# Performance work log

Measured on AMD Instinct MI355X. Metric: run time of the kernel, lower is better.

The kernel has to match this reference:

```python
import jax, jax.numpy as jnp
import numpy as np

EPS = 1e-6
H, A, V = 4, 64, 64  # heads, attn_dim, hidden_dim


def layer_norm(x, w, b):
    mu = jnp.mean(x, axis=-1, keepdims=True)
    var = jnp.var(x, axis=-1, keepdims=True)
    return (x - mu) * jax.lax.rsqrt(var + EPS) * w + b


def setup_inputs() -> dict:
    key = jax.random.key(0)
    B, N, D = 4, 2048, 512
    lengths = np.array([2048, 1536, 1024, 1792], np.int32)
    offsets = np.concatenate([[0], np.cumsum(lengths)]).astype(np.int32)
    L = int(offsets[-1])  # 6400
    uvqk_out = (2 * V + 2 * A) * H  # 1024
    out_in = 2 * V * H + D          # concat([u, x, normed_attn])
    ks = jax.random.split(key, 4)
    return {
        "x": jax.random.normal(ks[0], (L, D), jnp.float32),
        "x_lengths": jnp.asarray(lengths),
        "x_offsets": jnp.asarray(offsets),
        "max_seq_len": N,
        "num_targets": jnp.asarray([32, 16, 8, 64], jnp.int32),
        "uvqk_weight": jax.random.normal(ks[1], (D, uvqk_out), jnp.float32) / np.float32(np.sqrt(D)),
        "uvqk_bias": jnp.zeros((uvqk_out,), jnp.float32),
        "input_norm_weight": jnp.ones((D,), jnp.float32),
        "input_norm_bias": jnp.zeros((D,), jnp.float32),
        "output_norm_weight": jnp.ones((V * H,), jnp.float32),
        "output_norm_bias": jnp.zeros((V * H,), jnp.float32),
        "output_weight": jax.random.normal(ks[2], (out_in, D), jnp.float32) / np.float32(np.sqrt(out_in)),
    }


def reference(x, x_lengths, x_offsets, max_seq_len, num_targets,
              uvqk_weight, uvqk_bias, input_norm_weight, input_norm_bias,
              output_norm_weight, output_norm_bias, output_weight):
    L, D = x.shape
    B = x_lengths.shape[0]
    N = int(max_seq_len)
    alpha = A ** -0.5

    # fused input layernorm + UVQK projection + silu
    nx = layer_norm(x, input_norm_weight, input_norm_bias)
    uvqk = jax.nn.silu(nx @ uvqk_weight + uvqk_bias)              # [L, (2V+2A)*H]
    u = uvqk[:, : V * H]                                          # [L, V*H]
    v = uvqk[:, V * H: 2 * V * H].reshape(L, H, V)
    q = uvqk[:, 2 * V * H: 2 * V * H + A * H].reshape(L, H, A)
    k = uvqk[:, 2 * V * H + A * H:].reshape(L, H, A)

    # jagged -> padded [B, N, ...]
    pos = jnp.arange(N)
    gather_idx = jnp.clip(x_offsets[:-1, None] + pos[None, :], 0, L - 1)  # [B,N]
    valid = pos[None, :] < x_lengths[:, None]                              # [B,N]
    qp = q[gather_idx] * valid[..., None, None]
    kp = k[gather_idx] * valid[..., None, None]
    vp = v[gather_idx] * valid[..., None, None]

    # target-aware causal mask: clamp ids at uih boundary; eye | dist>0
    max_ids = (x_lengths - num_targets)[:, None]        # [B,1]
    ids = jnp.minimum(pos[None, :], max_ids)            # [B,N]
    dist = ids[:, :, None] - ids[:, None, :]            # [B,N,N]
    mask = (dist > 0) | jnp.eye(N, dtype=bool)[None]
    mask = mask & valid[:, :, None] & valid[:, None, :]

    scores = jnp.einsum("bnha,bmha->bhnm", qp, kp) * alpha
    attn_w = jax.nn.silu(scores) * (1.0 / N)
    attn_w = attn_w * mask[:, None].astype(attn_w.dtype)
    attn_p = jnp.einsum("bhnm,bmhv->bnhv", attn_w, vp).reshape(B, N, H * V)

    # padded -> jagged
    tok = jnp.arange(L)
    b_of = jnp.searchsorted(x_offsets, tok, side="right") - 1
    p_of = tok - x_offsets[b_of]
    attn = attn_p[b_of, p_of]                            # [L, H*V]

    # output: norm(attn), concat [u, x, y], project, residual (dropout off / eval)
    y = layer_norm(attn, output_norm_weight, output_norm_bias)
    y = jnp.concatenate([u, x, y], axis=1)
    return x + y @ output_weight
```

## Files before the change

kernel.cpp:

```cpp
#include <hip/hip_runtime.h>
#include <math.h>

#define NSEQ 2048
#define PIT 72
#define GP 40

typedef __attribute__((ext_vector_type(8))) short short8;
typedef __attribute__((ext_vector_type(4))) short short4v;
typedef __attribute__((ext_vector_type(4))) float f32x4;

__device__ __forceinline__ float silu_f(float z) {
    return z * __builtin_amdgcn_rcpf(1.f + __expf(-z));
}

__device__ __forceinline__ unsigned short f2bf(float f) {
    unsigned int u = __float_as_uint(f);
    u += 0x7fffu + ((u >> 16) & 1u);
    return (unsigned short)(u >> 16);
}

__device__ __forceinline__ unsigned short f2bf_fast(float f) {
    return (unsigned short)((__float_as_uint(f) + 0x8000u) >> 16);
}

__device__ __forceinline__ short8 scale8_pow2(short8 v, float s) {
    short8 r;
    #pragma unroll
    for (int i = 0; i < 8; i++) {
        float f = __uint_as_float(((unsigned int)(unsigned short)v[i]) << 16) * s;
        r[i] = (short)(unsigned short)(__float_as_uint(f) >> 16);
    }
    return r;
}

__global__ void __launch_bounds__(256) transpose_to_bf16(
    const float* __restrict__ W, unsigned short* __restrict__ Wt, int R, int C)
{
    __shared__ float t[32][33];
    int tid = threadIdx.x;
    int tr = tid >> 5, tc = tid & 31;
    int r0 = blockIdx.y * 32, c0 = blockIdx.x * 32;
    #pragma unroll
    for (int p = 0; p < 4; p++)
        t[tr + p * 8][tc] = W[(size_t)(r0 + tr + p * 8) * C + c0 + tc];
    __syncthreads();
    #pragma unroll
    for (int p = 0; p < 4; p++)
        Wt[(size_t)(c0 + tr + p * 8) * R + r0 + tc] = f2bf(t[tc][tr + p * 8]);
}

__global__ void __launch_bounds__(256) ln512_kernel(
    const float* __restrict__ x, const float* __restrict__ w,
    const float* __restrict__ b,
    unsigned short* __restrict__ nxb, unsigned short* __restrict__ A2)
{
    int row = blockIdx.x;
    int tid = threadIdx.x;
    const float* xr = x + (size_t)row * 512;
    float2 v = *(const float2*)(xr + tid * 2);
    float s = v.x + v.y;
    float sq = v.x * v.x + v.y * v.y;
    for (int o = 32; o > 0; o >>= 1) { s += __shfl_down(s, o); sq += __shfl_down(sq, o); }
    __shared__ float red[8];
    int wv = tid >> 6;
    if ((tid & 63) == 0) { red[wv] = s; red[4 + wv] = sq; }
    __syncthreads();
    float ts = red[0] + red[1] + red[2] + red[3];
    float tq = red[4] + red[5] + red[6] + red[7];
    float mu = ts * (1.f / 512.f);
    float var = tq * (1.f / 512.f) - mu * mu;
    float rs = rsqrtf(var + 1e-6f);
    float2 wv2 = *(const float2*)(w + tid * 2);
    float2 bv  = *(const float2*)(b + tid * 2);
    ushort2 hn, hx;
    hn.x = f2bf((v.x - mu) * rs * wv2.x + bv.x);
    hn.y = f2bf((v.y - mu) * rs * wv2.y + bv.y);
    hx.x = f2bf(v.x);
    hx.y = f2bf(v.y);
    *(ushort2*)(nxb + (size_t)row * 512 + tid * 2) = hn;
    *(ushort2*)(A2 + (size_t)row * 1024 + 256 + tid * 2) = hx;
}

__global__ void __launch_bounds__(256) ln256_kernel(
    const float* __restrict__ a, const float* __restrict__ w,
    const float* __restrict__ b, unsigned short* __restrict__ A2)
{
    int row = blockIdx.x;
    int tid = threadIdx.x;
    float v = a[(size_t)row * 256 + tid];
    float s = v, sq = v * v;
    for (int o = 32; o > 0; o >>= 1) { s += __shfl_down(s, o); sq += __shfl_down(sq, o); }
    __shared__ float red[8];
    int wv = tid >> 6;
    if ((tid & 63) == 0) { red[wv] = s; red[4 + wv] = sq; }
    __syncthreads();
    float ts = red[0] + red[1] + red[2] + red[3];
    float tq = red[4] + red[5] + red[6] + red[7];
    float mu = ts * (1.f / 256.f);
    float var = tq * (1.f / 256.f) - mu * mu;
    float rs = rsqrtf(var + 1e-6f);
    A2[(size_t)row * 1024 + 768 + tid] = f2bf((v - mu) * rs * w[tid] + b[tid]);
}

__global__ void __launch_bounds__(256) gemm1_mfma(
    const unsigned short* __restrict__ Ab, const unsigned short* __restrict__ Bt,
    const float* __restrict__ bias,
    unsigned short* __restrict__ A2, unsigned short* __restrict__ qkvb)
{
    constexpr int K = 512, KIT = K / 32;
    __shared__ unsigned short As[2][128 * GP];
    __shared__ unsigned short Bs[2][64 * GP];
    int tid = threadIdx.x, lane = tid & 63, w = tid >> 6;
    int nn = lane & 15, qd = lane >> 4;
    int bm = blockIdx.y * 128, bn = blockIdx.x * 64;
    int arow = tid >> 1, aseg = (tid & 1) * 16;
    int brow = tid >> 2, bseg = (tid & 3) * 8;
    const unsigned short* Ag = Ab + (size_t)(bm + arow) * K + aseg;
    const unsigned short* Bg = Bt + (size_t)(bn + brow) * K + bseg;

    short8 pa0 = *(const short8*)Ag;
    short8 pa1 = *(const short8*)(Ag + 8);
    short8 pb0 = *(const short8*)Bg;

    f32x4 acc[2][4];
    #pragma unroll
    for (int i = 0; i < 2; i++)
        #pragma unroll
        for (int j = 0; j < 4; j++) acc[i][j] = (f32x4){0.f, 0.f, 0.f, 0.f};

    int buf = 0;
    for (int it = 0; it < KIT; ++it) {
        *(short8*)&As[buf][arow * GP + aseg]     = pa0;
        *(short8*)&As[buf][arow * GP + aseg + 8] = pa1;
        *(short8*)&Bs[buf][brow * GP + bseg]     = pb0;
        __syncthreads();
        if (it + 1 < KIT) {
            int k0 = (it + 1) * 32;
            pa0 = *(const short8*)(Ag + k0);
            pa1 = *(const short8*)(Ag + k0 + 8);
            pb0 = *(const short8*)(Bg + k0);
        }
        short8 af[2], bf[4];
        #pragma unroll
        for (int i = 0; i < 2; i++)
            af[i] = *(const short8*)&As[buf][(w * 32 + i * 16 + nn) * GP + qd * 8];
        #pragma unroll
        for (int j = 0; j < 4; j++)
            bf[j] = *(const short8*)&Bs[buf][(j * 16 + nn) * GP + qd * 8];
        #pragma unroll
        for (int i = 0; i < 2; i++)
            #pragma unroll
            for (int j = 0; j < 4; j++)
                acc[i][j] = __builtin_amdgcn_mfma_f32_16x16x32_bf16(af[i], bf[j], acc[i][j], 0, 0, 0);
        buf ^= 1;
    }
    bool isU = (bn < 256);
    #pragma unroll
    for (int j = 0; j < 4; j++) {
        int col = bn + j * 16 + nn;
        float bb = bias[col];
        #pragma unroll
        for (int i = 0; i < 2; i++) {
            int rbase = bm + w * 32 + i * 16 + qd * 4;
            #pragma unroll
            for (int r = 0; r < 4; r++) {
                unsigned short hh = f2bf(silu_f(acc[i][j][r] + bb));
                if (isU) A2[(size_t)(rbase + r) * 1024 + col] = hh;
                else     qkvb[(size_t)(rbase + r) * 768 + col - 256] = hh;
            }
        }
    }
}

__global__ void __launch_bounds__(256) gemm2_mfma(
    const unsigned short* __restrict__ Ab, const unsigned short* __restrict__ Bt,
    const float* __restrict__ x, float* __restrict__ out)
{
    constexpr int K = 1024, KIT = K / 32;
    __shared__ unsigned short As[2][128 * GP];
    __shared__ unsigned short Bs[2][64 * GP];
    int tid = threadIdx.x, lane = tid & 63, w = tid >> 6;
    int nn = lane & 15, qd = lane >> 4;
    int bm = blockIdx.y * 128, bn = blockIdx.x * 64;
    int arow = tid >> 1, aseg = (tid & 1) * 16;
    int brow = tid >> 2, bseg = (tid & 3) * 8;
    const unsigned short* Ag = Ab + (size_t)(bm + arow) * K + aseg;
    const unsigned short* Bg = Bt + (size_t)(bn + brow) * K + bseg;

    short8 pa0 = *(const short8*)Ag;
    short8 pa1 = *(const short8*)(Ag + 8);
    short8 pb0 = *(const short8*)Bg;

    f32x4 acc[2][4];
    #pragma unroll
    for (int i = 0; i < 2; i++)
        #pragma unroll
        for (int j = 0; j < 4; j++) acc[i][j] = (f32x4){0.f, 0.f, 0.f, 0.f};

    int buf = 0;
    for (int it = 0; it < KIT; ++it) {
        *(short8*)&As[buf][arow * GP + aseg]     = pa0;
        *(short8*)&As[buf][arow * GP + aseg + 8] = pa1;
        *(short8*)&Bs[buf][brow * GP + bseg]     = pb0;
        __syncthreads();
        if (it + 1 < KIT) {
            int k0 = (it + 1) * 32;
            pa0 = *(const short8*)(Ag + k0);
            pa1 = *(const short8*)(Ag + k0 + 8);
            pb0 = *(const short8*)(Bg + k0);
        }
        short8 af[2], bf[4];
        #pragma unroll
        for (int i = 0; i < 2; i++)
            af[i] = *(const short8*)&As[buf][(w * 32 + i * 16 + nn) * GP + qd * 8];
        #pragma unroll
        for (int j = 0; j < 4; j++)
            bf[j] = *(const short8*)&Bs[buf][(j * 16 + nn) * GP + qd * 8];
        #pragma unroll
        for (int i = 0; i < 2; i++)
            #pragma unroll
            for (int j = 0; j < 4; j++)
                acc[i][j] = __builtin_amdgcn_mfma_f32_16x16x32_bf16(af[i], bf[j], acc[i][j], 0, 0, 0);
        buf ^= 1;
    }
    #pragma unroll
    for (int j = 0; j < 4; j++) {
        int col = bn + j * 16 + nn;
        #pragma unroll
        for (int i = 0; i < 2; i++) {
            int rbase = bm + w * 32 + i * 16 + qd * 4;
            #pragma unroll
            for (int r = 0; r < 4; r++) {
                size_t idx = (size_t)(rbase + r) * 512 + col;
                out[idx] = x[idx] + acc[i][j][r];
            }
        }
    }
}

__global__ void __launch_bounds__(256, 2) attn_mfma_kernel(
    const unsigned short* __restrict__ qkvb,
    const int* __restrict__ offsets,
    const int* __restrict__ lengths,
    const int* __restrict__ num_targets,
    float* __restrict__ attn)
{
    int bh = blockIdx.y;
    int b = bh >> 2, h = bh & 3;
    int len = lengths[b];
    int n0 = (31 - (int)blockIdx.x) * 64;
    if (n0 >= len) return;
    int m_hi = min(n0 + 63, len - 1);
    int off = offsets[b];
    int max_id = len - num_targets[b];
    int tid = threadIdx.x, lane = tid & 63, w = tid >> 6;
    int nn = lane & 15, qd = lane >> 4;

    __shared__ __align__(16) char smem[69632];
    unsigned short* Vt = (unsigned short*)(smem + w * 9216);
    float* Os = (float*)smem;

    short8 qf[4][2];
    #pragma unroll
    for (int g = 0; g < 4; g++) {
        int row = min(n0 + g * 16 + nn, len - 1);
        const unsigned short* base = qkvb + (size_t)(off + row) * 768 + 256 + h * 64;
        qf[g][0] = scale8_pow2(*(const short8*)(base + qd * 8), 0.125f);
        qf[g][1] = scale8_pow2(*(const short8*)(base + 32 + qd * 8), 0.125f);
    }

    f32x4 o_acc[4][4];
    #pragma unroll
    for (int t = 0; t < 4; t++)
        #pragma unroll
        for (int g = 0; g < 4; g++) o_acc[t][g] = (f32x4){0.f, 0.f, 0.f, 0.f};

    int fast_lim = min(n0, max_id);
    int r0 = (lane & 15) * 4, d0 = (lane >> 4) * 16;

    short8 kf[4][2], kn[4][2], vf[4][2];
    int m_first = w * 64;
    if (m_first <= m_hi) {
        #pragma unroll
        for (int s = 0; s < 4; s++) {
            int row = min(m_first + s * 16 + nn, len - 1);
            const unsigned short* kb = qkvb + (size_t)(off + row) * 768 + 512 + h * 64 + qd * 8;
            kf[s][0] = *(const short8*)kb;
            kf[s][1] = *(const short8*)(kb + 32);
        }
        #pragma unroll
        for (int j = 0; j < 4; j++) {
            int row = min(m_first + r0 + j, len - 1);
            const unsigned short* vb = qkvb + (size_t)(off + row) * 768 + h * 64 + d0;
            vf[j][0] = *(const short8*)vb;
            vf[j][1] = *(const short8*)(vb + 8);
        }
    }

    for (int m0 = m_first; m0 <= m_hi; m0 += 256) {
        #pragma unroll
        for (int dd = 0; dd < 16; dd++) {
            int hh = dd >> 3, e = dd & 7;
            short4v pk;
            pk[0] = vf[0][hh][e]; pk[1] = vf[1][hh][e];
            pk[2] = vf[2][hh][e]; pk[3] = vf[3][hh][e];
            *(short4v*)&Vt[(d0 + dd) * PIT + r0] = pk;
        }
        int mnext = m0 + 256;
        if (mnext <= m_hi) {
            #pragma unroll
            for (int j = 0; j < 4; j++) {
                int row = min(mnext + r0 + j, len - 1);
                const unsigned short* vb = qkvb + (size_t)(off + row) * 768 + h * 64 + d0;
                vf[j][0] = *(const short8*)vb;
                vf[j][1] = *(const short8*)(vb + 8);
            }
            #pragma unroll
            for (int s = 0; s < 4; s++) {
                int row = min(mnext + s * 16 + nn, len - 1);
                const unsigned short* kb = qkvb + (size_t)(off + row) * 768 + 512 + h * 64 + qd * 8;
                kn[s][0] = *(const short8*)kb;
                kn[s][1] = *(const short8*)(kb + 32);
            }
        }
        bool fastp = (m0 + 63 < fast_lim);
        #pragma unroll
        for (int s = 0; s < 4; s++) {
            f32x4 st[4];
            #pragma unroll
            for (int g = 0; g < 4; g++) {
                st[g] = (f32x4){0.f, 0.f, 0.f, 0.f};
                st[g] = __builtin_amdgcn_mfma_f32_16x16x32_bf16(kf[s][0], qf[g][0], st[g], 0, 0, 0);
                st[g] = __builtin_amdgcn_mfma_f32_16x16x32_bf16(kf[s][1], qf[g][1], st[g], 0, 0, 0);
            }
            short4v bop[4];
            if (fastp) {
                #pragma unroll
                for (int g = 0; g < 4; g++)
                    #pragma unroll
                    for (int r = 0; r < 4; r++)
                        bop[g][r] = (short)f2bf_fast(silu_f(st[g][r]));
            } else {
                #pragma unroll
                for (int g = 0; g < 4; g++) {
                    int nc_ = n0 + g * 16 + nn;
                    int id_ = min(nc_, max_id);
                    #pragma unroll
                    for (int r = 0; r < 4; r++) {
                        int mcol = m0 + s * 16 + qd * 4 + r;
                        bool ok = (mcol < id_) || (mcol == nc_);
                        bop[g][r] = (short)f2bf_fast(ok ? silu_f(st[g][r]) : 0.f);
                    }
                }
            }
            #pragma unroll
            for (int t = 0; t < 4; t++) {
                short4v aop = *(const short4v*)&Vt[(t * 16 + nn) * PIT + s * 16 + qd * 4];
                #pragma unroll
                for (int g = 0; g < 4; g++)
                    o_acc[t][g] = __builtin_amdgcn_mfma_f32_16x16x16bf16_1k(aop, bop[g], o_acc[t][g], 0, 0, 0);
            }
        }
        if (mnext <= m_hi) {
            #pragma unroll
            for (int s = 0; s < 4; s++) { kf[s][0] = kn[s][0]; kf[s][1] = kn[s][1]; }
        }
    }

    __syncthreads();
    const float invN = 1.f / (float)NSEQ;
    float* Ow = Os + w * 4352;
    #pragma unroll
    for (int t = 0; t < 4; t++)
        #pragma unroll
        for (int g = 0; g < 4; g++) {
            f32x4 v = o_acc[t][g] * invN;
            *(f32x4*)&Ow[(g * 16 + nn) * 68 + t * 16 + qd * 4] = v;
        }
    __syncthreads();
    int rr = tid >> 2, cs = (tid & 3) * 16;
    if (n0 + rr < len) {
        float* dst = attn + (size_t)(off + n0 + rr) * 256 + h * 64 + cs;
        #pragma unroll
        for (int q4 = 0; q4 < 4; q4++) {
            f32x4 v = (f32x4){0.f, 0.f, 0.f, 0.f};
            #pragma unroll
            for (int w2 = 0; w2 < 4; w2++)
                v += *(const f32x4*)&Os[w2 * 4352 + rr * 68 + cs + q4 * 4];
            *(f32x4*)(dst + q4 * 4) = v;
        }
    }
}

extern "C" void kernel_launch(void* const* d_in, const int* in_sizes, int n_in,
                              void* d_out, int out_size, void* d_ws, size_t ws_size,
                              hipStream_t stream)
{
    const float* x          = (const float*)d_in[0];
    const int*   x_lengths  = (const int*)d_in[1];
    const int*   x_offsets  = (const int*)d_in[2];
    const int*   num_targets = (const int*)d_in[4];
    const float* uvqk_w     = (const float*)d_in[5];
    const float* uvqk_b     = (const float*)d_in[6];
    const float* in_w       = (const float*)d_in[7];
    const float* in_b       = (const float*)d_in[8];
    const float* out_w      = (const float*)d_in[9];
    const float* out_b      = (const float*)d_in[10];
    const float* Wo         = (const float*)d_in[11];
    float* out = (float*)d_out;

    int L = in_sizes[0] / 512;
    int B = in_sizes[1];

    char* ws = (char*)d_ws;
    size_t o = 0;
    float* attn = (float*)(ws + o);          o += (size_t)L * 256 * 4;
    unsigned short* nxb  = (unsigned short*)(ws + o); o += (size_t)L * 512 * 2;
    unsigned short* A2   = (unsigned short*)(ws + o); o += (size_t)L * 1024 * 2;
    unsigned short* qkvb = (unsigned short*)(ws + o); o += (size_t)L * 768 * 2;
    unsigned short* W1t  = (unsigned short*)(ws + o); o += (size_t)1024 * 512 * 2;
    unsigned short* W2t  = (unsigned short*)(ws + o); o += (size_t)512 * 1024 * 2;

    transpose_to_bf16<<<dim3(1024 / 32, 512 / 32), 256, 0, stream>>>(uvqk_w, W1t, 512, 1024);
    transpose_to_bf16<<<dim3(512 / 32, 1024 / 32), 256, 0, stream>>>(Wo, W2t, 1024, 512);

    ln512_kernel<<<L, 256, 0, stream>>>(x, in_w, in_b, nxb, A2);

    dim3 g1(1024 / 64, L / 128);
    gemm1_mfma<<<g1, 256, 0, stream>>>(nxb, W1t, uvqk_b, A2, qkvb);

    dim3 g2(NSEQ / 64, 16);
    attn_mfma_kernel<<<g2, 256, 0, stream>>>(qkvb, x_offsets, x_lengths, num_targets, attn);

    ln256_kernel<<<L, 256, 0, stream>>>(attn, out_w, out_b, A2);

    dim3 g3(512 / 64, L / 128);
    gemm2_mfma<<<g3, 256, 0, stream>>>(A2, W2t, x, out);
}
```

Before: 178.9 us.

## Retile GEMMs to 64x128 with K=64 steps and vectorize layernorm rows

Both MFMA GEMMs change from 128x64 tiles with K-step 32 and double-buffered LDS to 64x128 tiles with a 2x2 wave grid, K-step 64 and a single LDS buffer guarded by two barriers per iteration. This halves the number of K iterations and barriers and changes per-wave reuse of the A and B fragments. Separately, both layernorm kernels now process two rows per block with wider vector loads. The single buffer adds a barrier before each store, and the tile counts change occupancy and grid shape: the gemm2 grid stays at 400 blocks, while gemm1 grows from 800 to 800 blocks (same count, different shape).

```diff
diff --git a/kernel.cpp b/kernel.cpp
--- a/kernel.cpp
+++ b/kernel.cpp
@@ -3,7 +3,6 @@
 
 #define NSEQ 2048
 #define PIT 72
-#define GP 40
 
 typedef __attribute__((ext_vector_type(8))) short short8;
 typedef __attribute__((ext_vector_type(4))) short short4v;
@@ -54,52 +53,61 @@
     const float* __restrict__ b,
     unsigned short* __restrict__ nxb, unsigned short* __restrict__ A2)
 {
-    int row = blockIdx.x;
     int tid = threadIdx.x;
-    const float* xr = x + (size_t)row * 512;
-    float2 v = *(const float2*)(xr + tid * 2);
-    float s = v.x + v.y;
-    float sq = v.x * v.x + v.y * v.y;
+    int r = tid >> 7;
+    int row = blockIdx.x * 2 + r;
+    int c = (tid & 127) * 4;
+    float4 v = *(const float4*)(x + (size_t)row * 512 + c);
+    float s = v.x + v.y + v.z + v.w;
+    float sq = v.x * v.x + v.y * v.y + v.z * v.z + v.w * v.w;
     for (int o = 32; o > 0; o >>= 1) { s += __shfl_down(s, o); sq += __shfl_down(sq, o); }
     __shared__ float red[8];
     int wv = tid >> 6;
     if ((tid & 63) == 0) { red[wv] = s; red[4 + wv] = sq; }
     __syncthreads();
-    float ts = red[0] + red[1] + red[2] + red[3];
-    float tq = red[4] + red[5] + red[6] + red[7];
+    float ts = red[2 * r] + red[2 * r + 1];
+    float tq = red[4 + 2 * r] + red[4 + 2 * r + 1];
     float mu = ts * (1.f / 512.f);
     float var = tq * (1.f / 512.f) - mu * mu;
     float rs = rsqrtf(var + 1e-6f);
-    float2 wv2 = *(const float2*)(w + tid * 2);
-    float2 bv  = *(const float2*)(b + tid * 2);
-    ushort2 hn, hx;
-    hn.x = f2bf((v.x - mu) * rs * wv2.x + bv.x);
-    hn.y = f2bf((v.y - mu) * rs * wv2.y + bv.y);
-    hx.x = f2bf(v.x);
-    hx.y = f2bf(v.y);
-    *(ushort2*)(nxb + (size_t)row * 512 + tid * 2) = hn;
-    *(ushort2*)(A2 + (size_t)row * 1024 + 256 + tid * 2) = hx;
+    float4 wv4 = *(const float4*)(w + c);
+    float4 bv4 = *(const float4*)(b + c);
+    ushort4 hn, hx;
+    hn.x = f2bf((v.x - mu) * rs * wv4.x + bv4.x);
+    hn.y = f2bf((v.y - mu) * rs * wv4.y + bv4.y);
+    hn.z = f2bf((v.z - mu) * rs * wv4.z + bv4.z);
+    hn.w = f2bf((v.w - mu) * rs * wv4.w + bv4.w);
+    hx.x = f2bf(v.x); hx.y = f2bf(v.y); hx.z = f2bf(v.z); hx.w = f2bf(v.w);
+    *(ushort4*)(nxb + (size_t)row * 512 + c) = hn;
+    *(ushort4*)(A2 + (size_t)row * 1024 + 256 + c) = hx;
 }
 
 __global__ void __launch_bounds__(256) ln256_kernel(
     const float* __restrict__ a, const float* __restrict__ w,
     const float* __restrict__ b, unsigned short* __restrict__ A2)
 {
-    int row = blockIdx.x;
     int tid = threadIdx.x;
-    float v = a[(size_t)row * 256 + tid];
-    float s = v, sq = v * v;
+    int r = tid >> 7;
+    int row = blockIdx.x * 2 + r;
+    int c = (tid & 127) * 2;
+    float2 v = *(const float2*)(a + (size_t)row * 256 + c);
+    float s = v.x + v.y, sq = v.x * v.x + v.y * v.y;
     for (int o = 32; o > 0; o >>= 1) { s += __shfl_down(s, o); sq += __shfl_down(sq, o); }
     __shared__ float red[8];
     int wv = tid >> 6;
     if ((tid & 63) == 0) { red[wv] = s; red[4 + wv] = sq; }
     __syncthreads();
-    float ts = red[0] + red[1] + red[2] + red[3];
-    float tq = red[4] + red[5] + red[6] + red[7];
+    float ts = red[2 * r] + red[2 * r + 1];
+    float tq = red[4 + 2 * r] + red[4 + 2 * r + 1];
     float mu = ts * (1.f / 256.f);
     float var = tq * (1.f / 256.f) - mu * mu;
     float rs = rsqrtf(var + 1e-6f);
-    A2[(size_t)row * 1024 + 768 + tid] = f2bf((v - mu) * rs * w[tid] + b[tid]);
+    float2 w2 = *(const float2*)(w + c);
+    float2 b2 = *(const float2*)(b + c);
+    ushort2 h;
+    h.x = f2bf((v.x - mu) * rs * w2.x + b2.x);
+    h.y = f2bf((v.y - mu) * rs * w2.y + b2.y);
+    *(ushort2*)(A2 + (size_t)row * 1024 + 768 + c) = h;
 }
 
 __global__ void __launch_bounds__(256) gemm1_mfma(
@@ -107,20 +115,21 @@
     const float* __restrict__ bias,
     unsigned short* __restrict__ A2, unsigned short* __restrict__ qkvb)
 {
-    constexpr int K = 512, KIT = K / 32;
-    __shared__ unsigned short As[2][128 * GP];
-    __shared__ unsigned short Bs[2][64 * GP];
+    constexpr int K = 512, KIT = K / 64;
+    __shared__ unsigned short As[64 * PIT];
+    __shared__ unsigned short Bs[128 * PIT];
     int tid = threadIdx.x, lane = tid & 63, w = tid >> 6;
+    int wr = w >> 1, wc = w & 1;
     int nn = lane & 15, qd = lane >> 4;
-    int bm = blockIdx.y * 128, bn = blockIdx.x * 64;
-    int arow = tid >> 1, aseg = (tid & 1) * 16;
-    int brow = tid >> 2, bseg = (tid & 3) * 8;
-    const unsigned short* Ag = Ab + (size_t)(bm + arow) * K + aseg;
-    const unsigned short* Bg = Bt + (size_t)(bn + brow) * K + bseg;
-
-    short8 pa0 = *(const short8*)Ag;
-    short8 pa1 = *(const short8*)(Ag + 8);
-    short8 pb0 = *(const short8*)Bg;
+    int bm = blockIdx.y * 64, bn = blockIdx.x * 128;
+    int arow = tid >> 2, ac0 = (tid & 3) * 16;
+    int brow = tid >> 1, bc0 = (tid & 1) * 32;
+    const unsigned short* Ag = Ab + (size_t)(bm + arow) * K + ac0;
+    const unsigned short* Bg = Bt + (size_t)(bn + brow) * K + bc0;
+
+    short8 pa0 = *(const short8*)Ag, pa1 = *(const short8*)(Ag + 8);
+    short8 pb0 = *(const short8*)Bg, pb1 = *(const short8*)(Bg + 8);
+    short8 pb2 = *(const short8*)(Bg + 16), pb3 = *(const short8*)(Bg + 24);
 
     f32x4 acc[2][4];
     #pragma unroll
@@ -128,40 +137,45 @@
         #pragma unroll
         for (int j = 0; j < 4; j++) acc[i][j] = (f32x4){0.f, 0.f, 0.f, 0.f};
 
-    int buf = 0;
     for (int it = 0; it < KIT; ++it) {
-        *(short8*)&As[buf][arow * GP + aseg]     = pa0;
-        *(short8*)&As[buf][arow * GP + aseg + 8] = pa1;
-        *(short8*)&Bs[buf][brow * GP + bseg]     = pb0;
+        __syncthreads();
+        *(short8*)&As[arow * PIT + ac0]     = pa0;
+        *(short8*)&As[arow * PIT + ac0 + 8] = pa1;
+        *(short8*)&Bs[brow * PIT + bc0]      = pb0;
+        *(short8*)&Bs[brow * PIT + bc0 + 8]  = pb1;
+        *(short8*)&Bs[brow * PIT + bc0 + 16] = pb2;
+        *(short8*)&Bs[brow * PIT + bc0 + 24] = pb3;
         __syncthreads();
         if (it + 1 < KIT) {
-            int k0 = (it + 1) * 32;
-            pa0 = *(const short8*)(Ag + k0);
-            pa1 = *(const short8*)(Ag + k0 + 8);
-            pb0 = *(const short8*)(Bg + k0);
-        }
-        short8 af[2], bf[4];
-        #pragma unroll
-        for (int i = 0; i < 2; i++)
-            af[i] = *(const short8*)&As[buf][(w * 32 + i * 16 + nn) * GP + qd * 8];
-        #pragma unroll
-        for (int j = 0; j < 4; j++)
-            bf[j] = *(const short8*)&Bs[buf][(j * 16 + nn) * GP + qd * 8];
-        #pragma unroll
-        for (int i = 0; i < 2; i++)
+            int k0 = (it + 1) * 64;
+            pa0 = *(const short8*)(Ag + k0); pa1 = *(const short8*)(Ag + k0 + 8);
+            pb0 = *(const short8*)(Bg + k0); pb1 = *(const short8*)(Bg + k0 + 8);
+            pb2 = *(const short8*)(Bg + k0 + 16); pb3 = *(const short8*)(Bg + k0 + 24);
+        }
+        #pragma unroll
+        for (int kk = 0; kk < 2; kk++) {
+            short8 af[2], bf[4];
+            #pragma unroll
+            for (int i = 0; i < 2; i++)
+                af[i] = *(const short8*)&As[(wr * 32 + i * 16 + nn) * PIT + kk * 32 + qd * 8];
             #pragma unroll
             for (int j = 0; j < 4; j++)
-                acc[i][j] = __builtin_amdgcn_mfma_f32_16x16x32_bf16(af[i], bf[j], acc[i][j], 0, 0, 0);
-        buf ^= 1;
+                bf[j] = *(const short8*)&Bs[(wc * 64 + j * 16 + nn) * PIT + kk * 32 + qd * 8];
+            #pragma unroll
+            for (int i = 0; i < 2; i++)
+                #pragma unroll
+                for (int j = 0; j < 4; j++)
+                    acc[i][j] = __builtin_amdgcn_mfma_f32_16x16x32_bf16(af[i], bf[j], acc[i][j], 0, 0, 0);
+        }
     }
     bool isU = (bn < 256);
     #pragma unroll
     for (int j = 0; j < 4; j++) {
-        int col = bn + j * 16 + nn;
+        int col = bn + wc * 64 + j * 16 + nn;
         float bb = bias[col];
         #pragma unroll
         for (int i = 0; i < 2; i++) {
-            int rbase = bm + w * 32 + i * 16 + qd * 4;
+            int rbase = bm + wr * 32 + i * 16 + qd * 4;
             #pragma unroll
             for (int r = 0; r < 4; r++) {
                 unsigned short hh = f2bf(silu_f(acc[i][j][r] + bb));
@@ -176,20 +190,21 @@
     const unsigned short* __restrict__ Ab, const unsigned short* __restrict__ Bt,
     const float* __restrict__ x, float* __restrict__ out)
 {
-    constexpr int K = 1024, KIT = K / 32;
-    __shared__ unsigned short As[2][128 * GP];
-    __shared__ unsigned short Bs[2][64 * GP];
+    constexpr int K = 1024, KIT = K / 64;
+    __shared__ unsigned short As[64 * PIT];
+    __shared__ unsigned short Bs[128 * PIT];
     int tid = threadIdx.x, lane = tid & 63, w = tid >> 6;
+    int wr = w >> 1, wc = w & 1;
     int nn = lane & 15, qd = lane >> 4;
-    int bm = blockIdx.y * 128, bn = blockIdx.x * 64;
-    int arow = tid >> 1, aseg = (tid & 1) * 16;
-    int brow = tid >> 2, bseg = (tid & 3) * 8;
-    const unsigned short* Ag = Ab + (size_t)(bm + arow) * K + aseg;
-    const unsigned short* Bg = Bt + (size_t)(bn + brow) * K + bseg;
-
-    short8 pa0 = *(const short8*)Ag;
-    short8 pa1 = *(const short8*)(Ag + 8);
-    short8 pb0 = *(const short8*)Bg;
+    int bm = blockIdx.y * 64, bn = blockIdx.x * 128;
+    int arow = tid >> 2, ac0 = (tid & 3) * 16;
+    int brow = tid >> 1, bc0 = (tid & 1) * 32;
+    const unsigned short* Ag = Ab + (size_t)(bm + arow) * K + ac0;
+    const unsigned short* Bg = Bt + (size_t)(bn + brow) * K + bc0;
+
+    short8 pa0 = *(const short8*)Ag, pa1 = *(const short8*)(Ag + 8);
+    short8 pb0 = *(const short8*)Bg, pb1 = *(const short8*)(Bg + 8);
+    short8 pb2 = *(const short8*)(Bg + 16), pb3 = *(const short8*)(Bg + 24);
 
     f32x4 acc[2][4];
     #pragma unroll
@@ -197,38 +212,43 @@
         #pragma unroll
         for (int j = 0; j < 4; j++) acc[i][j] = (f32x4){0.f, 0.f, 0.f, 0.f};
 
-    int buf = 0;
     for (int it = 0; it < KIT; ++it) {
-        *(short8*)&As[buf][arow * GP + aseg]     = pa0;
-        *(short8*)&As[buf][arow * GP + aseg + 8] = pa1;
-        *(short8*)&Bs[buf][brow * GP + bseg]     = pb0;
+        __syncthreads();
+        *(short8*)&As[arow * PIT + ac0]     = pa0;
+        *(short8*)&As[arow * PIT + ac0 + 8] = pa1;
+        *(short8*)&Bs[brow * PIT + bc0]      = pb0;
+        *(short8*)&Bs[brow * PIT + bc0 + 8]  = pb1;
+        *(short8*)&Bs[brow * PIT + bc0 + 16] = pb2;
+        *(short8*)&Bs[brow * PIT + bc0 + 24] = pb3;
         __syncthreads();
         if (it + 1 < KIT) {
-            int k0 = (it + 1) * 32;
-            pa0 = *(const short8*)(Ag + k0);
-            pa1 = *(const short8*)(Ag + k0 + 8);
-            pb0 = *(const short8*)(Bg + k0);
-        }
-        short8 af[2], bf[4];
-        #pragma unroll
-        for (int i = 0; i < 2; i++)
-            af[i] = *(const short8*)&As[buf][(w * 32 + i * 16 + nn) * GP + qd * 8];
-        #pragma unroll
-        for (int j = 0; j < 4; j++)
-            bf[j] = *(const short8*)&Bs[buf][(j * 16 + nn) * GP + qd * 8];
-        #pragma unroll
-        for (int i = 0; i < 2; i++)
+            int k0 = (it + 1) * 64;
+            pa0 = *(const short8*)(Ag + k0); pa1 = *(const short8*)(Ag + k0 + 8);
+            pb0 = *(const short8*)(Bg + k0); pb1 = *(const short8*)(Bg + k0 + 8);
+            pb2 = *(const short8*)(Bg + k0 + 16); pb3 = *(const short8*)(Bg + k0 + 24);
+        }
+        #pragma unroll
+        for (int kk = 0; kk < 2; kk++) {
+            short8 af[2], bf[4];
+            #pragma unroll
+            for (int i = 0; i < 2; i++)
+                af[i] = *(const short8*)&As[(wr * 32 + i * 16 + nn) * PIT + kk * 32 + qd * 8];
             #pragma unroll
             for (int j = 0; j < 4; j++)
-                acc[i][j] = __builtin_amdgcn_mfma_f32_16x16x32_bf16(af[i], bf[j], acc[i][j], 0, 0, 0);
-        buf ^= 1;
+                bf[j] = *(const short8*)&Bs[(wc * 64 + j * 16 + nn) * PIT + kk * 32 + qd * 8];
+            #pragma unroll
+            for (int i = 0; i < 2; i++)
+                #pragma unroll
+                for (int j = 0; j < 4; j++)
+                    acc[i][j] = __builtin_amdgcn_mfma_f32_16x16x32_bf16(af[i], bf[j], acc[i][j], 0, 0, 0);
+        }
     }
     #pragma unroll
     for (int j = 0; j < 4; j++) {
-        int col = bn + j * 16 + nn;
+        int col = bn + wc * 64 + j * 16 + nn;
         #pragma unroll
         for (int i = 0; i < 2; i++) {
-            int rbase = bm + w * 32 + i * 16 + qd * 4;
+            int rbase = bm + wr * 32 + i * 16 + qd * 4;
             #pragma unroll
             for (int r = 0; r < 4; r++) {
                 size_t idx = (size_t)(rbase + r) * 512 + col;
@@ -424,16 +444,16 @@
     transpose_to_bf16<<<dim3(1024 / 32, 512 / 32), 256, 0, stream>>>(uvqk_w, W1t, 512, 1024);
     transpose_to_bf16<<<dim3(512 / 32, 1024 / 32), 256, 0, stream>>>(Wo, W2t, 1024, 512);
 
-    ln512_kernel<<<L, 256, 0, stream>>>(x, in_w, in_b, nxb, A2);
-
-    dim3 g1(1024 / 64, L / 128);
+    ln512_kernel<<<L / 2, 256, 0, stream>>>(x, in_w, in_b, nxb, A2);
+
+    dim3 g1(1024 / 128, L / 64);
     gemm1_mfma<<<g1, 256, 0, stream>>>(nxb, W1t, uvqk_b, A2, qkvb);
 
     dim3 g2(NSEQ / 64, 16);
     attn_mfma_kernel<<<g2, 256, 0, stream>>>(qkvb, x_offsets, x_lengths, num_targets, attn);
 
-    ln256_kernel<<<L, 256, 0, stream>>>(attn, out_w, out_b, A2);
-
-    dim3 g3(512 / 64, L / 128);
+    ln256_kernel<<<L / 2, 256, 0, stream>>>(attn, out_w, out_b, A2);
+
+    dim3 g3(512 / 128, L / 64);
     gemm2_mfma<<<g3, 256, 0, stream>>>(A2, W2t, x, out);
 }
```

After: 170.7 us. -4.6%, faster.
